# Kernel optimization log

Hardware: AMD Instinct MI355X
Metric: run time of the kernel (lower is better)

The kernel has to match this reference:

```python
import jax, jax.numpy as jnp
import numpy as np

DIM = 768
NUM_HEADS = 16
D = DIM // NUM_HEADS  # 48


def setup_inputs() -> dict:
    key = jax.random.key(0)
    ks = jax.random.split(key, 7)
    x = jax.random.normal(ks[0], (4, 4096, DIM), dtype=jnp.float32)
    # Linear weights stored as [in, out] for x @ W + b
    s = 1.0 / np.sqrt(DIM)
    Wq = jax.random.uniform(ks[1], (DIM, D), jnp.float32, -s, s)
    Wk = jax.random.uniform(ks[2], (DIM, D), jnp.float32, -s, s)
    Wv = jax.random.uniform(ks[3], (DIM, D), jnp.float32, -s, s)
    bq = jax.random.uniform(ks[4], (D,), jnp.float32, -s, s)
    bk = jax.random.uniform(ks[5], (D,), jnp.float32, -s, s)
    bv = jax.random.uniform(ks[6], (D,), jnp.float32, -s, s)
    return {"x": x, "Wq": Wq, "bq": bq, "Wk": Wk, "bk": bk, "Wv": Wv, "bv": bv}


def reference(x, Wq, bq, Wk, bk, Wv, bv):
    # q, k, v: [B, S, D]
    q = x @ Wq + bq
    k = x @ Wk + bk
    v = x @ Wv + bv
    scale = 1.0 / jnp.sqrt(jnp.asarray(D, dtype=q.dtype))
    # scores: [B, S_q, S_k]
    scores = jnp.einsum("bqd,bkd->bqk", q, k) * scale
    # NOTE: softmax over dim=1 = the QUERY axis (faithful to original torch code)
    qk = jax.nn.softmax(scores, axis=1)
    # dropout is identity in eval mode (deterministic reference)
    attn = jnp.einsum("bqk,bkd->bqd", qk, v)
    return attn
```

## Files before the change

kernel.cpp:

```cpp
#include <hip/hip_runtime.h>
#include <hip/hip_bf16.h>

#define NB 4
#define SEQ 4096
#define CDIM 768
#define HD 48

typedef __attribute__((ext_vector_type(8))) __bf16 bf16x8;
typedef __attribute__((ext_vector_type(16))) float f32x16;

static constexpr float SCALE_LOG2E = 0.20823542135164923f;

__device__ __forceinline__ bf16x8 ldg8(const __hip_bfloat16* p) {
    uint4 u = *reinterpret_cast<const uint4*>(p);
    bf16x8 r;
    __builtin_memcpy(&r, &u, 16);
    return r;
}
__device__ __forceinline__ unsigned pk2(float lo, float hi) {
    const __hip_bfloat16 a = __float2bfloat16(lo);
    const __hip_bfloat16 b = __float2bfloat16(hi);
    unsigned short ua, ub;
    __builtin_memcpy(&ua, &a, 2);
    __builtin_memcpy(&ub, &b, 2);
    return (unsigned)ua | ((unsigned)ub << 16);
}
__device__ __forceinline__ bf16x8 mk8(unsigned w0, unsigned w1, unsigned w2, unsigned w3) {
    const uint4 u = make_uint4(w0, w1, w2, w3);
    bf16x8 r;
    __builtin_memcpy(&r, &u, 16);
    return r;
}
__device__ __forceinline__ void plswap(unsigned& a, unsigned& b) {
    asm volatile("v_permlane32_swap_b32 %0, %1" : "+v"(a), "+v"(b));
}
__device__ __forceinline__ size_t fragOff(int tile, int s, int h) {
    return (((size_t)tile * 3 + s) * 2 + h) * 256;
}
__device__ __forceinline__ void xcd_remap64(int id, int& b, int& st) {
    const int xcd = id & 7;
    b  = xcd >> 1;
    st = (xcd & 1) * 32 + (id >> 3);
}

__global__ __launch_bounds__(256) void prep_kernel(
    const float* __restrict__ Wq, const float* __restrict__ Wk,
    const float* __restrict__ Wv,
    const float* __restrict__ bq, const float* __restrict__ bk,
    const float* __restrict__ bv,
    __hip_bfloat16* __restrict__ Wf, float* __restrict__ bias)
{
    const int g = blockIdx.x * 256 + threadIdx.x;
    if (g < 15360) {
        const int rem  = g % 3072;
        const int nt   = g / 3072;
        const int ks   = rem >> 6;
        const int l2   = rem & 63;
        const int hh   = l2 >> 5;
        const int lane = l2 & 31;
        const int n    = nt * 32 + lane;
        const float* src = (n < 48) ? Wq : (n < 96) ? Wk : (n < 144) ? Wv : nullptr;
        const int col = (n < 48) ? n : (n < 96) ? (n - 48) : (n - 96);
        #pragma unroll
        for (int j = 0; j < 8; ++j) {
            const int k = ks * 16 + hh * 8 + j;
            const float wv = src ? src[(size_t)k * HD + col] : 0.0f;
            Wf[(size_t)g * 8 + j] = __float2bfloat16(wv);
        }
    }
    if (blockIdx.x == 0 && threadIdx.x < 160) {
        const int t = threadIdx.x;
        bias[t] = (t < 48) ? bq[t] : (t < 96) ? bk[t - 48] : (t < 144) ? bv[t - 96] : 0.0f;
    }
}

__global__ __launch_bounds__(320) void proj_kernel(
    const float* __restrict__ x,
    const __hip_bfloat16* __restrict__ Wf, const float* __restrict__ bias,
    __hip_bfloat16* __restrict__ Qf, __hip_bfloat16* __restrict__ Kf,
    float* __restrict__ Vf)
{
    __shared__ __hip_bfloat16 xs[48 * 512];

    const int t   = threadIdx.x;
    const int w   = t >> 6;
    const int l   = t & 63;
    const int lo5 = l & 31, h = l >> 5;
    const int mt  = blockIdx.x;
    const int m0  = mt * 32;

    const float* xb = x + (size_t)m0 * CDIM;
    #pragma unroll
    for (int i = 0; i < 20; ++i) {
        const int c = i * 320 + t;
        if (c < 6144) {
            const int r   = c / 192;
            const int pos = c % 192;
            const int k   = pos * 4;
            const float4 v = *reinterpret_cast<const float4*>(xb + (size_t)r * CDIM + k);
            const int ks = k >> 4, hh = (k >> 3) & 1, j = k & 7;
            const uint2 d = make_uint2(pk2(v.x, v.y), pk2(v.z, v.w));
            *reinterpret_cast<uint2*>(&xs[ks * 512 + (hh * 32 + r) * 8 + j]) = d;
        }
    }
    __syncthreads();

    const __hip_bfloat16* bp = Wf + (size_t)w * 24576 + l * 8;
    f32x16 acc = {};
    #pragma unroll 8
    for (int ks = 0; ks < 48; ++ks) {
        bf16x8 a;
        __builtin_memcpy(&a, &xs[ks * 512 + l * 8], 16);
        const bf16x8 b = ldg8(bp + (size_t)ks * 512);
        __builtin_amdgcn_s_setprio(1);
        acc = __builtin_amdgcn_mfma_f32_32x32x16_bf16(a, b, acc, 0, 0, 0);
        __builtin_amdgcn_s_setprio(0);
    }

    const int n_g = w * 32 + lo5;
    const float bs = bias[n_g];
    if (n_g < 96) {
        const bool isQ = (n_g < 48);
        const int d  = isQ ? n_g : n_g - 48;
        const int s  = d >> 4;
        const int hf = (d >> 3) & 1;
        __hip_bfloat16* base = (isQ ? Qf : Kf) + fragOff(mt, s, hf) + (d & 7);
        #pragma unroll
        for (int r = 0; r < 16; ++r) {
            const int mrow = (r & 3) + 8 * (r >> 2) + 4 * h;
            float val = acc[r] + bs;
            if (isQ) val *= SCALE_LOG2E;
            base[mrow * 8] = __float2bfloat16(val);
        }
    } else if (n_g < 144) {
        const int d = n_g - 96;
        #pragma unroll
        for (int r = 0; r < 16; ++r) {
            const int m = m0 + (r & 3) + 8 * (r >> 2) + 4 * h;
            Vf[(size_t)m * HD + d] = acc[r] + bs;
        }
    }
}

__global__ __launch_bounds__(512, 2) void stats_kernel(
    const __hip_bfloat16* __restrict__ Qf, const __hip_bfloat16* __restrict__ Kf,
    const float* __restrict__ Vf, __hip_bfloat16* __restrict__ Vt)
{
    __shared__ float part[8][64];
    __shared__ float linv[64];

    const int t   = threadIdx.x;
    const int w   = t >> 6;
    const int l   = t & 63;
    const int lo5 = l & 31, h = l >> 5;
    int b, kst;
    xcd_remap64(blockIdx.x, b, kst);
    const int ktile0 = b * 128 + kst * 2;

    bf16x8 ka[6];
    #pragma unroll
    for (int s = 0; s < 3; ++s) {
        ka[s]     = ldg8(Kf + fragOff(ktile0,     s, h) + lo5 * 8);
        ka[3 + s] = ldg8(Kf + fragOff(ktile0 + 1, s, h) + lo5 * 8);
    }

    float lsum[32];
    #pragma unroll
    for (int r = 0; r < 32; ++r) lsum[r] = 0.0f;

    const int qt0 = b * 128 + w * 16;
    #pragma unroll 2
    for (int qq = 0; qq < 16; ++qq) {
        bf16x8 qb[3];
        #pragma unroll
        for (int s = 0; s < 3; ++s)
            qb[s] = ldg8(Qf + fragOff(qt0 + qq, s, h) + lo5 * 8);
        f32x16 a0 = {}, a1 = {};
        __builtin_amdgcn_s_setprio(1);
        #pragma unroll
        for (int s = 0; s < 3; ++s)
            a0 = __builtin_amdgcn_mfma_f32_32x32x16_bf16(ka[s], qb[s], a0, 0, 0, 0);
        #pragma unroll
        for (int s = 0; s < 3; ++s)
            a1 = __builtin_amdgcn_mfma_f32_32x32x16_bf16(ka[3 + s], qb[s], a1, 0, 0, 0);
        __builtin_amdgcn_s_setprio(0);
        #pragma unroll
        for (int r = 0; r < 16; ++r) {
            lsum[r]      += __builtin_amdgcn_exp2f(a0[r]);
            lsum[16 + r] += __builtin_amdgcn_exp2f(a1[r]);
        }
    }

    #pragma unroll
    for (int r = 0; r < 32; ++r) {
        lsum[r] += __shfl_xor(lsum[r], 1);
        lsum[r] += __shfl_xor(lsum[r], 2);
        lsum[r] += __shfl_xor(lsum[r], 4);
        lsum[r] += __shfl_xor(lsum[r], 8);
        lsum[r] += __shfl_xor(lsum[r], 16);
    }
    if (lo5 == 0) {
        #pragma unroll
        for (int r = 0; r < 16; ++r) {
            const int row = (r & 3) + 8 * (r >> 2) + 4 * h;
            part[w][row]      = lsum[r];
            part[w][32 + row] = lsum[16 + r];
        }
    }
    __syncthreads();
    if (t < 64) {
        float s = 0.0f;
        #pragma unroll
        for (int p = 0; p < 8; ++p) s += part[p][t];
        linv[t] = 1.0f / s;
    }
    __syncthreads();

    const int kp = t & 15;
    const int dg = t >> 4;
    #pragma unroll
    for (int tt = 0; tt < 2; ++tt) {
        const int ktile = ktile0 + tt;
        const float f0 = linv[tt * 32 + 2 * kp], f1 = linv[tt * 32 + 2 * kp + 1];
        __hip_bfloat16* vtb = Vt + (size_t)ktile * 2048;
        const float* vfb = Vf + ((size_t)b * SEQ + (kst * 2 + tt) * 32 + 2 * kp) * HD;
        {
            const int d = dg;
            const float v0 = vfb[d], v1 = vfb[HD + d];
            *reinterpret_cast<unsigned*>(&vtb[d * 32 + 2 * kp]) = pk2(v0 * f0, v1 * f1);
        }
        if (dg < 16) {
            const int d = dg + 32;
            const float v0 = vfb[d], v1 = vfb[HD + d];
            *reinterpret_cast<unsigned*>(&vtb[d * 32 + 2 * kp]) = pk2(v0 * f0, v1 * f1);
        }
    }
}

__global__ __launch_bounds__(512, 2) void pv_kernel(
    const __hip_bfloat16* __restrict__ Qf, const __hip_bfloat16* __restrict__ Kf,
    const __hip_bfloat16* __restrict__ Vt, float* __restrict__ out)
{
    __shared__ float red[8][32][64];

    const int t   = threadIdx.x;
    const int w   = t >> 6;
    const int l   = t & 63;
    const int lo5 = l & 31, h = l >> 5;
    int b, qst;
    xcd_remap64(blockIdx.x, b, qst);
    const int qtile0 = b * 128 + qst * 2;
    const int q0     = qst * 64;

    bf16x8 qb[6];
    #pragma unroll
    for (int s = 0; s < 3; ++s) {
        qb[s]     = ldg8(Qf + fragOff(qtile0,     s, h) + lo5 * 8);
        qb[3 + s] = ldg8(Qf + fragOff(qtile0 + 1, s, h) + lo5 * 8);
    }

    f32x16 o00 = {}, o01 = {}, o10 = {}, o11 = {};
    const int kt0 = b * 128 + w * 16;

    #pragma unroll 2
    for (int kk = 0; kk < 16; ++kk) {
        const int ktg = kt0 + kk;
        bf16x8 ka[3];
        #pragma unroll
        for (int s = 0; s < 3; ++s)
            ka[s] = ldg8(Kf + fragOff(ktg, s, h) + lo5 * 8);
        const __hip_bfloat16* vt = Vt + (size_t)ktg * 2048 + lo5 * 32 + 8 * h;
        const bf16x8 va  = ldg8(vt);
        const bf16x8 vb2 = ldg8(vt + 16);
        const bf16x8 vc  = ldg8(vt + 1024);
        const bf16x8 vd  = ldg8(vt + 1024 + 16);

        #pragma unroll
        for (int qt = 0; qt < 2; ++qt) {
            f32x16 acc = {};
            __builtin_amdgcn_s_setprio(1);
            #pragma unroll
            for (int s = 0; s < 3; ++s)
                acc = __builtin_amdgcn_mfma_f32_32x32x16_bf16(
                    ka[s], qb[3 * qt + s], acc, 0, 0, 0);
            __builtin_amdgcn_s_setprio(0);

            float p[16];
            #pragma unroll
            for (int r = 0; r < 16; ++r) p[r] = __builtin_amdgcn_exp2f(acc[r]);

            unsigned w0 = pk2(p[0],  p[1]),  w1 = pk2(p[2],  p[3]);
            unsigned w2 = pk2(p[4],  p[5]),  w3 = pk2(p[6],  p[7]);
            unsigned w4 = pk2(p[8],  p[9]),  w5 = pk2(p[10], p[11]);
            unsigned w6 = pk2(p[12], p[13]), w7 = pk2(p[14], p[15]);
            plswap(w0, w2);
            plswap(w1, w3);
            plswap(w4, w6);
            plswap(w5, w7);
            const bf16x8 pa0 = mk8(w0, w1, w2, w3);
            const bf16x8 pa1 = mk8(w4, w5, w6, w7);

            __builtin_amdgcn_s_setprio(1);
            if (qt == 0) {
                o00 = __builtin_amdgcn_mfma_f32_32x32x16_bf16(pa0, va,  o00, 0, 0, 0);
                o00 = __builtin_amdgcn_mfma_f32_32x32x16_bf16(pa1, vb2, o00, 0, 0, 0);
                o01 = __builtin_amdgcn_mfma_f32_32x32x16_bf16(pa0, vc,  o01, 0, 0, 0);
                o01 = __builtin_amdgcn_mfma_f32_32x32x16_bf16(pa1, vd,  o01, 0, 0, 0);
            } else {
                o10 = __builtin_amdgcn_mfma_f32_32x32x16_bf16(pa0, va,  o10, 0, 0, 0);
                o10 = __builtin_amdgcn_mfma_f32_32x32x16_bf16(pa1, vb2, o10, 0, 0, 0);
                o11 = __builtin_amdgcn_mfma_f32_32x32x16_bf16(pa0, vc,  o11, 0, 0, 0);
                o11 = __builtin_amdgcn_mfma_f32_32x32x16_bf16(pa1, vd,  o11, 0, 0, 0);
            }
            __builtin_amdgcn_s_setprio(0);
        }
    }

    #pragma unroll
    for (int round = 0; round < 2; ++round) {
        const f32x16& a = round ? o10 : o00;
        const f32x16& c = round ? o11 : o01;
        #pragma unroll
        for (int r = 0; r < 16; ++r) {
            red[w][r][l]      = a[r];
            red[w][16 + r][l] = c[r];
        }
        __syncthreads();
        {
            const int rr = t >> 4;
            const int l0 = (t & 15) * 4;
            float4 s = make_float4(0.f, 0.f, 0.f, 0.f);
            #pragma unroll
            for (int p = 0; p < 8; ++p) {
                const float4 v = *reinterpret_cast<const float4*>(&red[p][rr][l0]);
                s.x += v.x; s.y += v.y; s.z += v.z; s.w += v.w;
            }
            const int r    = rr & 15;
            const int row  = (r & 3) + 8 * (r >> 2) + 4 * (l0 >> 5);
            const int qrow = q0 + round * 32 + row;
            if (rr < 16) {
                *reinterpret_cast<float4*>(
                    &out[((size_t)(b * SEQ) + qrow) * HD + (l0 & 31)]) = s;
            } else if ((l0 & 31) < 16) {
                *reinterpret_cast<float4*>(
                    &out[((size_t)(b * SEQ) + qrow) * HD + 32 + (l0 & 31)]) = s;
            }
        }
        __syncthreads();
    }
}

extern "C" void kernel_launch(void* const* d_in, const int* in_sizes, int n_in,
                              void* d_out, int out_size, void* d_ws, size_t ws_size,
                              hipStream_t stream)
{
    const float* x  = (const float*)d_in[0];
    const float* Wq = (const float*)d_in[1];
    const float* bq = (const float*)d_in[2];
    const float* Wk = (const float*)d_in[3];
    const float* bk = (const float*)d_in[4];
    const float* Wv = (const float*)d_in[5];
    const float* bv = (const float*)d_in[6];
    float* out = (float*)d_out;

    const size_t FRAG = (size_t)512 * 6 * 256;
    __hip_bfloat16* Qf  = (__hip_bfloat16*)d_ws;
    __hip_bfloat16* Kf  = Qf + FRAG;
    float*          Vf  = (float*)(Kf + FRAG);
    __hip_bfloat16* Vt  = (__hip_bfloat16*)(Vf + (size_t)NB * SEQ * HD);
    __hip_bfloat16* Wf  = Vt + (size_t)NB * 128 * 2048;
    float*          bias = (float*)(Wf + (size_t)5 * 48 * 512);

    prep_kernel<<<dim3(60), 256, 0, stream>>>(Wq, Wk, Wv, bq, bk, bv, Wf, bias);
    proj_kernel<<<dim3(512), 320, 0, stream>>>(x, Wf, bias, Qf, Kf, Vf);
    stats_kernel<<<dim3(256), 512, 0, stream>>>(Qf, Kf, Vf, Vt);
    pv_kernel<<<dim3(256), 512, 0, stream>>>(Qf, Kf, Vt, out);
}
```

Before: 65.51 us.

## Software-pipeline global loads in projection, column-sum and attention kernels

```diff
diff --git a/kernel.cpp b/kernel.cpp
--- a/kernel.cpp
+++ b/kernel.cpp
@@ -80,7 +80,7 @@
     __hip_bfloat16* __restrict__ Qf, __hip_bfloat16* __restrict__ Kf,
     float* __restrict__ Vf)
 {
-    __shared__ __hip_bfloat16 xs[48 * 512];
+    __shared__ __hip_bfloat16 xs[2][24 * 512];
 
     const int t   = threadIdx.x;
     const int w   = t >> 6;
@@ -91,16 +91,23 @@
 
     const float* xb = x + (size_t)m0 * CDIM;
     #pragma unroll
-    for (int i = 0; i < 20; ++i) {
+    for (int i = 0; i < 10; ++i) {
         const int c = i * 320 + t;
-        if (c < 6144) {
-            const int r   = c / 192;
-            const int pos = c % 192;
-            const int k   = pos * 4;
-            const float4 v = *reinterpret_cast<const float4*>(xb + (size_t)r * CDIM + k);
-            const int ks = k >> 4, hh = (k >> 3) & 1, j = k & 7;
-            const uint2 d = make_uint2(pk2(v.x, v.y), pk2(v.z, v.w));
-            *reinterpret_cast<uint2*>(&xs[ks * 512 + (hh * 32 + r) * 8 + j]) = d;
+        if (c < 3072) {
+            const int r = c / 96, pos = c % 96;
+            const float4 v = *reinterpret_cast<const float4*>(xb + (size_t)r * CDIM + pos * 4);
+            const int ksl = pos >> 2, hh = (pos >> 1) & 1, j = (pos & 1) * 4;
+            *reinterpret_cast<uint2*>(&xs[0][ksl * 512 + (hh * 32 + r) * 8 + j]) =
+                make_uint2(pk2(v.x, v.y), pk2(v.z, v.w));
+        }
+    }
+    float4 stg[10];
+    #pragma unroll
+    for (int i = 0; i < 10; ++i) {
+        const int c = i * 320 + t;
+        if (c < 3072) {
+            const int r = c / 96, pos = c % 96;
+            stg[i] = *reinterpret_cast<const float4*>(xb + (size_t)r * CDIM + 384 + pos * 4);
         }
     }
     __syncthreads();
@@ -108,13 +115,30 @@
     const __hip_bfloat16* bp = Wf + (size_t)w * 24576 + l * 8;
     f32x16 acc = {};
     #pragma unroll 8
-    for (int ks = 0; ks < 48; ++ks) {
+    for (int ks = 0; ks < 24; ++ks) {
         bf16x8 a;
-        __builtin_memcpy(&a, &xs[ks * 512 + l * 8], 16);
+        __builtin_memcpy(&a, &xs[0][ks * 512 + l * 8], 16);
         const bf16x8 b = ldg8(bp + (size_t)ks * 512);
-        __builtin_amdgcn_s_setprio(1);
         acc = __builtin_amdgcn_mfma_f32_32x32x16_bf16(a, b, acc, 0, 0, 0);
-        __builtin_amdgcn_s_setprio(0);
+    }
+
+    #pragma unroll
+    for (int i = 0; i < 10; ++i) {
+        const int c = i * 320 + t;
+        if (c < 3072) {
+            const int r = c / 96, pos = c % 96;
+            const int ksl = pos >> 2, hh = (pos >> 1) & 1, j = (pos & 1) * 4;
+            *reinterpret_cast<uint2*>(&xs[1][ksl * 512 + (hh * 32 + r) * 8 + j]) =
+                make_uint2(pk2(stg[i].x, stg[i].y), pk2(stg[i].z, stg[i].w));
+        }
+    }
+    __syncthreads();
+    #pragma unroll 8
+    for (int ks = 0; ks < 24; ++ks) {
+        bf16x8 a;
+        __builtin_memcpy(&a, &xs[1][ks * 512 + l * 8], 16);
+        const bf16x8 b = ldg8(bp + (size_t)(24 + ks) * 512);
+        acc = __builtin_amdgcn_mfma_f32_32x32x16_bf16(a, b, acc, 0, 0, 0);
     }
 
     const int n_g = w * 32 + lo5;
@@ -169,20 +193,27 @@
     for (int r = 0; r < 32; ++r) lsum[r] = 0.0f;
 
     const int qt0 = b * 128 + w * 16;
-    #pragma unroll 2
+    bf16x8 qb[2][3];
+    #pragma unroll
+    for (int s = 0; s < 3; ++s)
+        qb[0][s] = ldg8(Qf + fragOff(qt0, s, h) + lo5 * 8);
+
+    #pragma unroll
     for (int qq = 0; qq < 16; ++qq) {
-        bf16x8 qb[3];
-        #pragma unroll
-        for (int s = 0; s < 3; ++s)
-            qb[s] = ldg8(Qf + fragOff(qt0 + qq, s, h) + lo5 * 8);
+        const int cur = qq & 1;
+        if (qq < 15) {
+            #pragma unroll
+            for (int s = 0; s < 3; ++s)
+                qb[cur ^ 1][s] = ldg8(Qf + fragOff(qt0 + qq + 1, s, h) + lo5 * 8);
+        }
         f32x16 a0 = {}, a1 = {};
         __builtin_amdgcn_s_setprio(1);
         #pragma unroll
         for (int s = 0; s < 3; ++s)
-            a0 = __builtin_amdgcn_mfma_f32_32x32x16_bf16(ka[s], qb[s], a0, 0, 0, 0);
+            a0 = __builtin_amdgcn_mfma_f32_32x32x16_bf16(ka[s], qb[cur][s], a0, 0, 0, 0);
         #pragma unroll
         for (int s = 0; s < 3; ++s)
-            a1 = __builtin_amdgcn_mfma_f32_32x32x16_bf16(ka[3 + s], qb[s], a1, 0, 0, 0);
+            a1 = __builtin_amdgcn_mfma_f32_32x32x16_bf16(ka[3 + s], qb[cur][s], a1, 0, 0, 0);
         __builtin_amdgcn_s_setprio(0);
         #pragma unroll
         for (int r = 0; r < 16; ++r) {
@@ -262,18 +293,32 @@
     f32x16 o00 = {}, o01 = {}, o10 = {}, o11 = {};
     const int kt0 = b * 128 + w * 16;
 
-    #pragma unroll 2
+    bf16x8 ka[2][3], vv[2][4];
+    {
+        #pragma unroll
+        for (int s = 0; s < 3; ++s)
+            ka[0][s] = ldg8(Kf + fragOff(kt0, s, h) + lo5 * 8);
+        const __hip_bfloat16* vt = Vt + (size_t)kt0 * 2048 + lo5 * 32 + 8 * h;
+        vv[0][0] = ldg8(vt);
+        vv[0][1] = ldg8(vt + 16);
+        vv[0][2] = ldg8(vt + 1024);
+        vv[0][3] = ldg8(vt + 1024 + 16);
+    }
+
+    #pragma unroll
     for (int kk = 0; kk < 16; ++kk) {
-        const int ktg = kt0 + kk;
-        bf16x8 ka[3];
-        #pragma unroll
-        for (int s = 0; s < 3; ++s)
-            ka[s] = ldg8(Kf + fragOff(ktg, s, h) + lo5 * 8);
-        const __hip_bfloat16* vt = Vt + (size_t)ktg * 2048 + lo5 * 32 + 8 * h;
-        const bf16x8 va  = ldg8(vt);
-        const bf16x8 vb2 = ldg8(vt + 16);
-        const bf16x8 vc  = ldg8(vt + 1024);
-        const bf16x8 vd  = ldg8(vt + 1024 + 16);
+        const int cur = kk & 1;
+        if (kk < 15) {
+            const int ktn = kt0 + kk + 1;
+            #pragma unroll
+            for (int s = 0; s < 3; ++s)
+                ka[cur ^ 1][s] = ldg8(Kf + fragOff(ktn, s, h) + lo5 * 8);
+            const __hip_bfloat16* vtn = Vt + (size_t)ktn * 2048 + lo5 * 32 + 8 * h;
+            vv[cur ^ 1][0] = ldg8(vtn);
+            vv[cur ^ 1][1] = ldg8(vtn + 16);
+            vv[cur ^ 1][2] = ldg8(vtn + 1024);
+            vv[cur ^ 1][3] = ldg8(vtn + 1024 + 16);
+        }
 
         #pragma unroll
         for (int qt = 0; qt < 2; ++qt) {
@@ -282,7 +327,7 @@
             #pragma unroll
             for (int s = 0; s < 3; ++s)
                 acc = __builtin_amdgcn_mfma_f32_32x32x16_bf16(
-                    ka[s], qb[3 * qt + s], acc, 0, 0, 0);
+                    ka[cur][s], qb[3 * qt + s], acc, 0, 0, 0);
             __builtin_amdgcn_s_setprio(0);
 
             float p[16];
@@ -302,15 +347,15 @@
 
             __builtin_amdgcn_s_setprio(1);
             if (qt == 0) {
-                o00 = __builtin_amdgcn_mfma_f32_32x32x16_bf16(pa0, va,  o00, 0, 0, 0);
-                o00 = __builtin_amdgcn_mfma_f32_32x32x16_bf16(pa1, vb2, o00, 0, 0, 0);
-                o01 = __builtin_amdgcn_mfma_f32_32x32x16_bf16(pa0, vc,  o01, 0, 0, 0);
-                o01 = __builtin_amdgcn_mfma_f32_32x32x16_bf16(pa1, vd,  o01, 0, 0, 0);
+                o00 = __builtin_amdgcn_mfma_f32_32x32x16_bf16(pa0, vv[cur][0], o00, 0, 0, 0);
+                o00 = __builtin_amdgcn_mfma_f32_32x32x16_bf16(pa1, vv[cur][1], o00, 0, 0, 0);
+                o01 = __builtin_amdgcn_mfma_f32_32x32x16_bf16(pa0, vv[cur][2], o01, 0, 0, 0);
+                o01 = __builtin_amdgcn_mfma_f32_32x32x16_bf16(pa1, vv[cur][3], o01, 0, 0, 0);
             } else {
-                o10 = __builtin_amdgcn_mfma_f32_32x32x16_bf16(pa0, va,  o10, 0, 0, 0);
-                o10 = __builtin_amdgcn_mfma_f32_32x32x16_bf16(pa1, vb2, o10, 0, 0, 0);
-                o11 = __builtin_amdgcn_mfma_f32_32x32x16_bf16(pa0, vc,  o11, 0, 0, 0);
-                o11 = __builtin_amdgcn_mfma_f32_32x32x16_bf16(pa1, vd,  o11, 0, 0, 0);
+                o10 = __builtin_amdgcn_mfma_f32_32x32x16_bf16(pa0, vv[cur][0], o10, 0, 0, 0);
+                o10 = __builtin_amdgcn_mfma_f32_32x32x16_bf16(pa1, vv[cur][1], o10, 0, 0, 0);
+                o11 = __builtin_amdgcn_mfma_f32_32x32x16_bf16(pa0, vv[cur][2], o11, 0, 0, 0);
+                o11 = __builtin_amdgcn_mfma_f32_32x32x16_bf16(pa1, vv[cur][3], o11, 0, 0, 0);
             }
             __builtin_amdgcn_s_setprio(0);
         }
```

After: 77.48 us. 18.3% more time.

## Write V transposed in projection and apply column normalization inside PV

Applied to the files above, without the earlier changes.

```diff
diff --git a/kernel.cpp b/kernel.cpp
--- a/kernel.cpp
+++ b/kernel.cpp
@@ -78,7 +78,7 @@
     const float* __restrict__ x,
     const __hip_bfloat16* __restrict__ Wf, const float* __restrict__ bias,
     __hip_bfloat16* __restrict__ Qf, __hip_bfloat16* __restrict__ Kf,
-    float* __restrict__ Vf)
+    __hip_bfloat16* __restrict__ Vt)
 {
     __shared__ __hip_bfloat16 xs[48 * 512];
 
@@ -134,20 +134,20 @@
         }
     } else if (n_g < 144) {
         const int d = n_g - 96;
-        #pragma unroll
-        for (int r = 0; r < 16; ++r) {
-            const int m = m0 + (r & 3) + 8 * (r >> 2) + 4 * h;
-            Vf[(size_t)m * HD + d] = acc[r] + bs;
+        __hip_bfloat16* vtb = Vt + (size_t)mt * 2048 + d * 32;
+        #pragma unroll
+        for (int r = 0; r < 16; ++r) {
+            const int kloc = (r & 3) + 8 * (r >> 2) + 4 * h;
+            vtb[kloc] = __float2bfloat16(acc[r] + bs);
         }
     }
 }
 
 __global__ __launch_bounds__(512, 2) void stats_kernel(
     const __hip_bfloat16* __restrict__ Qf, const __hip_bfloat16* __restrict__ Kf,
-    const float* __restrict__ Vf, __hip_bfloat16* __restrict__ Vt)
+    float* __restrict__ linv_g)
 {
     __shared__ float part[8][64];
-    __shared__ float linv[64];
 
     const int t   = threadIdx.x;
     const int w   = t >> 6;
@@ -212,34 +212,14 @@
         float s = 0.0f;
         #pragma unroll
         for (int p = 0; p < 8; ++p) s += part[p][t];
-        linv[t] = 1.0f / s;
-    }
-    __syncthreads();
-
-    const int kp = t & 15;
-    const int dg = t >> 4;
-    #pragma unroll
-    for (int tt = 0; tt < 2; ++tt) {
-        const int ktile = ktile0 + tt;
-        const float f0 = linv[tt * 32 + 2 * kp], f1 = linv[tt * 32 + 2 * kp + 1];
-        __hip_bfloat16* vtb = Vt + (size_t)ktile * 2048;
-        const float* vfb = Vf + ((size_t)b * SEQ + (kst * 2 + tt) * 32 + 2 * kp) * HD;
-        {
-            const int d = dg;
-            const float v0 = vfb[d], v1 = vfb[HD + d];
-            *reinterpret_cast<unsigned*>(&vtb[d * 32 + 2 * kp]) = pk2(v0 * f0, v1 * f1);
-        }
-        if (dg < 16) {
-            const int d = dg + 32;
-            const float v0 = vfb[d], v1 = vfb[HD + d];
-            *reinterpret_cast<unsigned*>(&vtb[d * 32 + 2 * kp]) = pk2(v0 * f0, v1 * f1);
-        }
+        linv_g[(size_t)b * SEQ + kst * 64 + t] = 1.0f / s;
     }
 }
 
 __global__ __launch_bounds__(512, 2) void pv_kernel(
     const __hip_bfloat16* __restrict__ Qf, const __hip_bfloat16* __restrict__ Kf,
-    const __hip_bfloat16* __restrict__ Vt, float* __restrict__ out)
+    const __hip_bfloat16* __restrict__ Vt, const float* __restrict__ linv_g,
+    float* __restrict__ out)
 {
     __shared__ float red[8][32][64];
 
@@ -261,6 +241,7 @@
 
     f32x16 o00 = {}, o01 = {}, o10 = {}, o11 = {};
     const int kt0 = b * 128 + w * 16;
+    const float* lb = linv_g + (size_t)b * SEQ + w * 512;
 
     #pragma unroll 2
     for (int kk = 0; kk < 16; ++kk) {
@@ -274,6 +255,15 @@
         const bf16x8 vb2 = ldg8(vt + 16);
         const bf16x8 vc  = ldg8(vt + 1024);
         const bf16x8 vd  = ldg8(vt + 1024 + 16);
+
+        float4 li0 = *reinterpret_cast<const float4*>(lb + kk * 32 + 4 * h);
+        float4 li1 = *reinterpret_cast<const float4*>(lb + kk * 32 + 8 + 4 * h);
+        float4 li2 = *reinterpret_cast<const float4*>(lb + kk * 32 + 16 + 4 * h);
+        float4 li3 = *reinterpret_cast<const float4*>(lb + kk * 32 + 24 + 4 * h);
+        const float lia[16] = {li0.x, li0.y, li0.z, li0.w,
+                               li1.x, li1.y, li1.z, li1.w,
+                               li2.x, li2.y, li2.z, li2.w,
+                               li3.x, li3.y, li3.z, li3.w};
 
         #pragma unroll
         for (int qt = 0; qt < 2; ++qt) {
@@ -287,7 +277,8 @@
 
             float p[16];
             #pragma unroll
-            for (int r = 0; r < 16; ++r) p[r] = __builtin_amdgcn_exp2f(acc[r]);
+            for (int r = 0; r < 16; ++r)
+                p[r] = __builtin_amdgcn_exp2f(acc[r]) * lia[r];
 
             unsigned w0 = pk2(p[0],  p[1]),  w1 = pk2(p[2],  p[3]);
             unsigned w2 = pk2(p[4],  p[5]),  w3 = pk2(p[6],  p[7]);
@@ -366,13 +357,13 @@
     const size_t FRAG = (size_t)512 * 6 * 256;
     __hip_bfloat16* Qf  = (__hip_bfloat16*)d_ws;
     __hip_bfloat16* Kf  = Qf + FRAG;
-    float*          Vf  = (float*)(Kf + FRAG);
-    __hip_bfloat16* Vt  = (__hip_bfloat16*)(Vf + (size_t)NB * SEQ * HD);
+    __hip_bfloat16* Vt  = Kf + FRAG;
     __hip_bfloat16* Wf  = Vt + (size_t)NB * 128 * 2048;
     float*          bias = (float*)(Wf + (size_t)5 * 48 * 512);
+    float*          linv = bias + 160;
 
     prep_kernel<<<dim3(60), 256, 0, stream>>>(Wq, Wk, Wv, bq, bk, bv, Wf, bias);
-    proj_kernel<<<dim3(512), 320, 0, stream>>>(x, Wf, bias, Qf, Kf, Vf);
-    stats_kernel<<<dim3(256), 512, 0, stream>>>(Qf, Kf, Vf, Vt);
-    pv_kernel<<<dim3(256), 512, 0, stream>>>(Qf, Kf, Vt, out);
-}
+    proj_kernel<<<dim3(512), 320, 0, stream>>>(x, Wf, bias, Qf, Kf, Vt);
+    stats_kernel<<<dim3(256), 512, 0, stream>>>(Qf, Kf, linv);
+    pv_kernel<<<dim3(256), 512, 0, stream>>>(Qf, Kf, Vt, linv, out);
+}
```

New measurement: 65.80 us (median of 2 runs). About the same (+0.4%).
